# Kernel optimization log

Hardware: AMD Instinct MI355X
Metric: run time of the kernel (lower is better)

## Reference

```python
import jax, jax.numpy as jnp
import numpy as np

B, N, DQ, DK, DV = 8, 2048, 1024, 1024, 1024

def setup_inputs() -> dict:
    key = jax.random.key(0)
    kx, kq, kk, kv = jax.random.split(key, 4)
    x = jax.random.normal(kx, (B, N, DQ), dtype=jnp.float32)
    # nn.Linear(dim_q, dim_k, bias=False) weights: [out, in]
    s = 1.0 / np.sqrt(DQ)
    Wq = jax.random.uniform(kq, (DK, DQ), jnp.float32, -s, s)
    Wk = jax.random.uniform(kk, (DK, DQ), jnp.float32, -s, s)
    Wv = jax.random.uniform(kv, (DV, DQ), jnp.float32, -s, s)
    return {"x": x, "Wq": Wq, "Wk": Wk, "Wv": Wv}

def reference(x, Wq, Wk, Wv):
    batch, n, _ = x.shape
    q = jnp.einsum('bnd,kd->bnk', x, Wq)  # [B,n,DK]
    k = jnp.einsum('bnd,kd->bnk', x, Wk)  # [B,n,DK]
    v = jnp.einsum('bnd,vd->bnv', x, Wv)  # [B,n,DV]
    norm = 1.0 / jnp.sqrt(jnp.asarray(Wq.shape[0], jnp.float32))
    dist = jnp.einsum('bik,bjk->bij', q, k) * norm  # [B,n,n]
    causal = jnp.tril(jnp.ones((n, n), dtype=bool))
    dist = jnp.where(causal[None, :, :], dist, jnp.float32(-1e20))
    dist = jax.nn.softmax(dist, axis=-1)
    att = jnp.einsum('bij,bjv->biv', dist, v)  # [B,n,DV]
    return att
```

## Files before the change

### kernel.cpp

```cpp
#include <hip/hip_runtime.h>
#include <hip/hip_bf16.h>

#define BM 128
#define BN 128
#define BK 32
#define TILE_ELEMS (BM * BK)

typedef __attribute__((ext_vector_type(4))) float floatx4;
typedef __bf16 bf16x8 __attribute__((ext_vector_type(8)));
typedef unsigned int u32;
typedef unsigned short u16;

typedef __attribute__((address_space(1))) const u32 g_u32;
typedef __attribute__((address_space(3))) u32 l_u32;

__device__ __forceinline__ u16 f32_to_bf16(float f) {
    union { float f; u32 u; } x{f};
    u32 u = x.u;
    u32 r = (u + 0x7fffu + ((u >> 16) & 1u)) >> 16;
    return (u16)r;
}


__device__ __forceinline__ void stage_half_sw(const u16* gbase, u16* lds_half, int tid) {
    int lane = tid & 63;
    int rsub = lane >> 3;
    int colsw = ((lane & 7) ^ rsub) << 3;
#pragma unroll
    for (int j = 0; j < 2; ++j) {
        int q = (tid >> 6) * 2 + j;
        int row = q * 8 + rsub;
        const u16* g = gbase + row * 1024 + colsw;
        u16* l = lds_half + q * 512 + lane * 8;
        __builtin_amdgcn_global_load_lds((g_u32*)g, (l_u32*)l, 16, 0, 0);
    }
}

__global__ __launch_bounds__(512, 2)
void qkv_gemm8(const u16* __restrict__ A, const u16* __restrict__ Bw, u16* __restrict__ C)
{
    __shared__ u16 As[2][256 * 64];
    __shared__ u16 Bs[2][256 * 64];

    int bid = blockIdx.x;
    int wg = (bid & 7) * 96 + (bid >> 3);
    int mt = wg / 12, nt = wg - mt * 12;

    int tid = threadIdx.x;
    int lane = tid & 63, wv = tid >> 6;
    int wr = wv >> 2, wc = wv & 3;
    int lrow = lane & 15, quad = lane >> 4;
    int sw = lrow & 7;

    const u16* Ab = A + (long)mt * 256 * 1024;
    const u16* Bb = Bw + (long)nt * 256 * 1024;

    stage_half_sw(Bb,                  &Bs[0][0],        tid);
    stage_half_sw(Bb + 128 * 1024,     &Bs[0][128 * 64], tid);
    stage_half_sw(Ab,                  &As[0][0],        tid);
    stage_half_sw(Ab + 128 * 1024,     &As[0][128 * 64], tid);
    stage_half_sw(Bb + 64,             &Bs[1][0],        tid);
    stage_half_sw(Bb + 64 + 128 * 1024,&Bs[1][128 * 64], tid);
    asm volatile("s_waitcnt vmcnt(4)" ::: "memory");
    __builtin_amdgcn_sched_barrier(0);
    __builtin_amdgcn_s_barrier();

    floatx4 acc[8][4] = {};

    const int arow = (wr * 128 + lrow) * 64;
    const int brow = (wc * 64 + lrow) * 64;
    const int sl0 = (quad ^ sw) * 8;
    const int sl1 = ((4 + quad) ^ sw) * 8;

    for (int i = 0; i < 8; ++i) {
        int t1  = 2 * i + 1;
        int tn  = (2 * i + 2 <= 15) ? 2 * i + 2 : 15;
        int tn1 = (2 * i + 3 <= 15) ? 2 * i + 3 : 15;
        const u16* gA1 = Ab + t1 * 64;
        const u16* gB2 = Bb + tn * 64;
        const u16* gA2 = Ab + tn * 64;
        const u16* gB3 = Bb + tn1 * 64;

        bf16x8 bq0[4], bq1[4];
#pragma unroll
        for (int half = 0; half < 2; ++half) {
#pragma unroll
            for (int p = 0; p < 4; ++p) {
                if (p == 0) {
#pragma unroll
                    for (int ni = 0; ni < 4; ++ni) {
                        bq0[ni] = *(const bf16x8*)&Bs[half][brow + ni * 1024 + sl0];
                        bq1[ni] = *(const bf16x8*)&Bs[half][brow + ni * 1024 + sl1];
                    }
                }
                bf16x8 a00 = *(const bf16x8*)&As[half][arow + (2 * p)     * 1024 + sl0];
                bf16x8 a01 = *(const bf16x8*)&As[half][arow + (2 * p)     * 1024 + sl1];
                bf16x8 a10 = *(const bf16x8*)&As[half][arow + (2 * p + 1) * 1024 + sl0];
                bf16x8 a11 = *(const bf16x8*)&As[half][arow + (2 * p + 1) * 1024 + sl1];

                int ph = half * 4 + p;
                switch (ph) {
                    case 0: stage_half_sw(gA1,              &As[1][0],        tid); break;
                    case 1: stage_half_sw(gA1 + 128 * 1024, &As[1][128 * 64], tid); break;
                    case 2: stage_half_sw(gB2,              &Bs[0][0],        tid); break;
                    case 3: stage_half_sw(gB2 + 128 * 1024, &Bs[0][128 * 64], tid); break;
                    case 4: stage_half_sw(gA2,              &As[0][0],        tid); break;
                    case 5: stage_half_sw(gA2 + 128 * 1024, &As[0][128 * 64], tid); break;
                    case 6: stage_half_sw(gB3,              &Bs[1][0],        tid); break;
                    case 7: stage_half_sw(gB3 + 128 * 1024, &Bs[1][128 * 64], tid); break;
                }

                __builtin_amdgcn_s_barrier();
                __builtin_amdgcn_s_setprio(1);
                int m0 = 2 * p;
#pragma unroll
                for (int ni = 0; ni < 4; ++ni) {
                    acc[m0][ni]     = __builtin_amdgcn_mfma_f32_16x16x32_bf16(a00, bq0[ni], acc[m0][ni],     0, 0, 0);
                    acc[m0][ni]     = __builtin_amdgcn_mfma_f32_16x16x32_bf16(a01, bq1[ni], acc[m0][ni],     0, 0, 0);
                    acc[m0 + 1][ni] = __builtin_amdgcn_mfma_f32_16x16x32_bf16(a10, bq0[ni], acc[m0 + 1][ni], 0, 0, 0);
                    acc[m0 + 1][ni] = __builtin_amdgcn_mfma_f32_16x16x32_bf16(a11, bq1[ni], acc[m0 + 1][ni], 0, 0, 0);
                }
                __builtin_amdgcn_s_setprio(0);
                if (p == 3) {
                    asm volatile("s_waitcnt vmcnt(4)" ::: "memory");
                    __builtin_amdgcn_sched_barrier(0);
                }
                __builtin_amdgcn_s_barrier();
            }
        }
    }
    asm volatile("s_waitcnt vmcnt(0)" ::: "memory");
    __builtin_amdgcn_sched_barrier(0);

    long crow0 = (long)mt * 256 + wr * 128 + quad * 4;
    int  ccol0 = nt * 256 + wc * 64 + lrow;
#pragma unroll
    for (int mi = 0; mi < 8; ++mi) {
#pragma unroll
        for (int r = 0; r < 4; ++r) {
            long row = crow0 + mi * 16 + r;
#pragma unroll
            for (int ni = 0; ni < 4; ++ni) {
                int col = ccol0 + ni * 16;
                C[row * 3072 + col] = f32_to_bf16(acc[mi][ni][r]);
            }
        }
    }
}


__device__ __forceinline__ void stage_tile(const u16* gbase, int ld, u16* lds, int tid) {
#pragma unroll
    for (int it = 0; it < 2; ++it) {
        int flat = it * 2048 + tid * 8;
        int row = flat >> 5;
        int col = flat & 31;
        const u16* g = gbase + (long)row * ld + col;
        __builtin_amdgcn_global_load_lds((g_u32*)g, (l_u32*)(&lds[flat]), 16, 0, 0);
    }
}

template<bool OUT_BF16, int MODE>
__device__ __forceinline__ void gemm_body(
    const u16* __restrict__ Ab, const u16* __restrict__ Bb, void* __restrict__ Cb,
    int lda, int ldb, long ldc, int m0, int n0, int nkt, float scale,
    u16* As, u16* Bs, float* lsum)
{
    int tid = threadIdx.x;

    const u16* Arow = Ab + (long)m0 * lda;
    const u16* Brow = Bb + (long)n0 * ldb;

    stage_tile(Arow, lda, As, tid);
    stage_tile(Brow, ldb, Bs, tid);

    int wave = tid >> 6, lane = tid & 63;
    int wr = (wave >> 1) * 64, wc = (wave & 1) * 64;
    int lrow = lane & 15, quad = lane >> 4;

    floatx4 acc[4][4] = {};
    const int aoff = (wr + lrow) * BK + quad * 8;
    const int boff = (wc + lrow) * BK + quad * 8;

    for (int kt = 0; kt < nkt; ++kt) {
        __syncthreads();
        bf16x8 af[4], bfr[4];
#pragma unroll
        for (int i = 0; i < 4; ++i) {
            af[i]  = *(const bf16x8*)&As[aoff + i * 16 * BK];
            bfr[i] = *(const bf16x8*)&Bs[boff + i * 16 * BK];
        }
#pragma unroll
        for (int mi = 0; mi < 4; ++mi)
#pragma unroll
            for (int ni = 0; ni < 4; ++ni)
                acc[mi][ni] = __builtin_amdgcn_mfma_f32_16x16x32_bf16(af[mi], bfr[ni], acc[mi][ni], 0, 0, 0);
        __syncthreads();
        if (kt + 1 < nkt) {
            stage_tile(Arow + (kt + 1) * BK, lda, As, tid);
            stage_tile(Brow + (kt + 1) * BK, ldb, Bs, tid);
        }
    }

    long crow0 = m0 + wr + quad * 4;
    int  ccol0 = n0 + wc + lrow;
#pragma unroll
    for (int mi = 0; mi < 4; ++mi) {
#pragma unroll
        for (int r = 0; r < 4; ++r) {
            long row = crow0 + mi * 16 + r;
            float rs = 0.f;
            float linv = 1.f;
            if (MODE == 2) linv = 1.0f / lsum[row];
#pragma unroll
            for (int ni = 0; ni < 4; ++ni) {
                long col = ccol0 + ni * 16;
                float v = acc[mi][ni][r] * scale;
                if (MODE == 1) {
                    float e = (col > row) ? 0.f : __expf(v);
                    ((u16*)Cb)[row * ldc + col] = f32_to_bf16(e);
                    rs += e;
                } else if (MODE == 2) {
                    ((float*)Cb)[row * ldc + col] = v * linv;
                } else {
                    if (OUT_BF16) ((u16*)Cb)[row * ldc + col] = f32_to_bf16(v);
                    else          ((float*)Cb)[row * ldc + col] = v;
                }
            }
            if (MODE == 1) {
                rs += __shfl_xor(rs, 1, 16);
                rs += __shfl_xor(rs, 2, 16);
                rs += __shfl_xor(rs, 4, 16);
                rs += __shfl_xor(rs, 8, 16);
                if (lrow == 0) atomicAdd(&lsum[row], rs);
            }
        }
    }
}

__global__ __launch_bounds__(256)
void s_gemm(const u16* __restrict__ QKVi, u16* __restrict__ P, float* __restrict__ lsum)
{
    __shared__ u16 As[TILE_ELEMS];
    __shared__ u16 Bs[TILE_ELEMS];
    int b = blockIdx.x, u = blockIdx.y, v = blockIdx.z;
    int mt, nt;
    if (u <= v) { mt = v; nt = u; } else { mt = 15 - v; nt = u - v - 1; }
    const u16* Ab = QKVi + (long)b * 2048 * 3072;
    const u16* Bb = Ab + 1024;
    gemm_body<true, 1>(Ab, Bb, P + (long)b * 2048 * 2048, 3072, 3072, 2048,
                       mt * BM, nt * BN, 32, 0.03125f, As, Bs, lsum + b * 2048);
}

__global__ __launch_bounds__(256)
void pv_gemm(const u16* __restrict__ P, const u16* __restrict__ Vt,
             float* __restrict__ O, const float* __restrict__ lsum)
{
    __shared__ u16 As[TILE_ELEMS];
    __shared__ u16 Bs[TILE_ELEMS];
    int b = blockIdx.x, nt = blockIdx.y, mt = blockIdx.z;
    const u16* Ab = P + (long)b * 2048 * 2048;
    const u16* Bb = Vt + (long)b * 2048;
    gemm_body<false, 2>(Ab, Bb, O + (long)b * 2048 * 1024, 2048, 16384, 1024,
                        mt * BM, nt * BN, mt * 4 + 4, 1.0f, As, Bs,
                        (float*)lsum + b * 2048);
}

__global__ __launch_bounds__(256)
void cvt_f32_bf16(const float* __restrict__ src, u16* __restrict__ dst, long n)
{
    long idx = ((long)blockIdx.x * 256 + threadIdx.x) << 2;
    if (idx >= n) return;
    float4 f = *(const float4*)(src + idx);
    ushort4 o;
    o.x = f32_to_bf16(f.x); o.y = f32_to_bf16(f.y);
    o.z = f32_to_bf16(f.z); o.w = f32_to_bf16(f.w);
    *(ushort4*)(dst + idx) = o;
}

__global__ __launch_bounds__(256)
void cvt_w3(const float* __restrict__ Wq, const float* __restrict__ Wk,
            const float* __restrict__ Wv, u16* __restrict__ dst)
{
    int which = blockIdx.x >> 10;
    const float* src = which == 0 ? Wq : (which == 1 ? Wk : Wv);
    long base = (long)(blockIdx.x & 1023) * 1024 + threadIdx.x * 4;
    float4 f = *(const float4*)(src + base);
    ushort4 o;
    o.x = f32_to_bf16(f.x); o.y = f32_to_bf16(f.y);
    o.z = f32_to_bf16(f.z); o.w = f32_to_bf16(f.w);
    *(ushort4*)(dst + (long)which * 1048576 + base) = o;
}

__global__ __launch_bounds__(256)
void transpose_v(const u16* __restrict__ QKVi, u16* __restrict__ Vt)
{
    __shared__ u16 tile[64][64 + 8];
    int t0 = blockIdx.x * 64;
    int d0 = blockIdx.y * 64;
    int tid = threadIdx.x;
    int lr = tid >> 3, lc = (tid & 7) * 8;
#pragma unroll
    for (int p = 0; p < 2; ++p) {
        int tok = lr + p * 32;
        const u16* src = QKVi + (long)(t0 + tok) * 3072 + 2048 + d0 + lc;
        *(uint4*)&tile[tok][lc] = *(const uint4*)src;
    }
    __syncthreads();
#pragma unroll
    for (int p = 0; p < 2; ++p) {
        int dq = lr + p * 32;
        u16 vals[8];
#pragma unroll
        for (int i = 0; i < 8; ++i) vals[i] = tile[lc + i][dq];
        *(uint4*)(Vt + (long)(d0 + dq) * 16384 + t0 + lc) = *(const uint4*)vals;
    }
}

extern "C" void kernel_launch(void* const* d_in, const int* in_sizes, int n_in,
                              void* d_out, int out_size, void* d_ws, size_t ws_size,
                              hipStream_t stream)
{
    const int B = 8, N = 2048, D = 1024;
    const long MT = (long)B * N;
    const long nX = MT * D;
    const long nW = (long)D * D;

    const float* x  = (const float*)d_in[0];
    const float* Wq = (const float*)d_in[1];
    const float* Wk = (const float*)d_in[2];
    const float* Wv = (const float*)d_in[3];
    float* out = (float*)d_out;

    u16* wb   = (u16*)d_ws;
    u16* xb   = wb + 3 * nW;
    u16* QKVi = xb + nX;
    u16* P    = QKVi + 3 * nX;
    u16* Vt   = xb;
    float* lsum = (float*)wb;

    cvt_f32_bf16<<<(int)(nX / 1024), 256, 0, stream>>>(x, xb, nX);
    cvt_w3<<<3072, 256, 0, stream>>>(Wq, Wk, Wv, wb);

    qkv_gemm8<<<dim3(768, 1, 1), 512, 0, stream>>>(xb, wb, QKVi);

    hipMemsetAsync(lsum, 0, (size_t)B * N * sizeof(float), stream);
    transpose_v<<<dim3(256, 16, 1), 256, 0, stream>>>(QKVi, Vt);

    s_gemm<<<dim3(8, 17, 8), 256, 0, stream>>>(QKVi, P, lsum);

    pv_gemm<<<dim3(8, 8, 16), 256, 0, stream>>>(P, Vt, out, lsum);
}
```

Baseline: 375.8 us.

## Fuse V transpose into QKV GEMM epilogue and widen PV GEMM tiles

The QKV projection GEMM now writes Q/K into a compact 2048-wide buffer and writes V directly in transposed layout from its accumulators. This removes the separate transpose_v kernel and its extra read/write pass over V. The PV GEMM is replaced with a 512-thread kernel using 128x256 tiles, dispatched with the heaviest causal row blocks first. That halves redundant reads of P per output column tile, at the cost of more LDS per block. The transposed V stores are strided 8-byte writes, which may coalesce poorly.

```diff
diff --git a/kernel.cpp b/kernel.cpp
--- a/kernel.cpp
+++ b/kernel.cpp
@@ -37,7 +37,8 @@
 }
 
 __global__ __launch_bounds__(512, 2)
-void qkv_gemm8(const u16* __restrict__ A, const u16* __restrict__ Bw, u16* __restrict__ C)
+void qkv_gemm8(const u16* __restrict__ A, const u16* __restrict__ Bw,
+               u16* __restrict__ QKi, u16* __restrict__ Vt)
 {
     __shared__ u16 As[2][256 * 64];
     __shared__ u16 Bs[2][256 * 64];
@@ -132,17 +133,32 @@
     asm volatile("s_waitcnt vmcnt(0)" ::: "memory");
     __builtin_amdgcn_sched_barrier(0);
 
-    long crow0 = (long)mt * 256 + wr * 128 + quad * 4;
-    int  ccol0 = nt * 256 + wc * 64 + lrow;
-#pragma unroll
-    for (int mi = 0; mi < 8; ++mi) {
-#pragma unroll
-        for (int r = 0; r < 4; ++r) {
-            long row = crow0 + mi * 16 + r;
+    if (nt < 8) {
+        long crow0 = (long)mt * 256 + wr * 128 + quad * 4;
+        int  ccol0 = nt * 256 + wc * 64 + lrow;
+#pragma unroll
+        for (int mi = 0; mi < 8; ++mi) {
+#pragma unroll
+            for (int r = 0; r < 4; ++r) {
+                long row = crow0 + mi * 16 + r;
+#pragma unroll
+                for (int ni = 0; ni < 4; ++ni)
+                    QKi[row * 2048 + ccol0 + ni * 16] = f32_to_bf16(acc[mi][ni][r]);
+            }
+        }
+    } else {
+        int dv0   = (nt - 8) * 256 + wc * 64 + lrow;
+        long tok0 = (long)mt * 256 + wr * 128 + quad * 4;
+#pragma unroll
+        for (int mi = 0; mi < 8; ++mi) {
 #pragma unroll
             for (int ni = 0; ni < 4; ++ni) {
-                int col = ccol0 + ni * 16;
-                C[row * 3072 + col] = f32_to_bf16(acc[mi][ni][r]);
+                ushort4 o;
+                o.x = f32_to_bf16(acc[mi][ni][0]);
+                o.y = f32_to_bf16(acc[mi][ni][1]);
+                o.z = f32_to_bf16(acc[mi][ni][2]);
+                o.w = f32_to_bf16(acc[mi][ni][3]);
+                *(ushort4*)(Vt + (long)(dv0 + ni * 16) * 16384 + tok0 + mi * 16) = o;
             }
         }
     }
@@ -210,8 +226,6 @@
         for (int r = 0; r < 4; ++r) {
             long row = crow0 + mi * 16 + r;
             float rs = 0.f;
-            float linv = 1.f;
-            if (MODE == 2) linv = 1.0f / lsum[row];
 #pragma unroll
             for (int ni = 0; ni < 4; ++ni) {
                 long col = ccol0 + ni * 16;
@@ -220,8 +234,6 @@
                     float e = (col > row) ? 0.f : __expf(v);
                     ((u16*)Cb)[row * ldc + col] = f32_to_bf16(e);
                     rs += e;
-                } else if (MODE == 2) {
-                    ((float*)Cb)[row * ldc + col] = v * linv;
                 } else {
                     if (OUT_BF16) ((u16*)Cb)[row * ldc + col] = f32_to_bf16(v);
                     else          ((float*)Cb)[row * ldc + col] = v;
@@ -239,31 +251,94 @@
 }
 
 __global__ __launch_bounds__(256)
-void s_gemm(const u16* __restrict__ QKVi, u16* __restrict__ P, float* __restrict__ lsum)
+void s_gemm(const u16* __restrict__ QKi, u16* __restrict__ P, float* __restrict__ lsum)
 {
     __shared__ u16 As[TILE_ELEMS];
     __shared__ u16 Bs[TILE_ELEMS];
     int b = blockIdx.x, u = blockIdx.y, v = blockIdx.z;
     int mt, nt;
     if (u <= v) { mt = v; nt = u; } else { mt = 15 - v; nt = u - v - 1; }
-    const u16* Ab = QKVi + (long)b * 2048 * 3072;
+    const u16* Ab = QKi + (long)b * 2048 * 2048;
     const u16* Bb = Ab + 1024;
-    gemm_body<true, 1>(Ab, Bb, P + (long)b * 2048 * 2048, 3072, 3072, 2048,
+    gemm_body<true, 1>(Ab, Bb, P + (long)b * 2048 * 2048, 2048, 2048, 2048,
                        mt * BM, nt * BN, 32, 0.03125f, As, Bs, lsum + b * 2048);
 }
 
-__global__ __launch_bounds__(256)
-void pv_gemm(const u16* __restrict__ P, const u16* __restrict__ Vt,
-             float* __restrict__ O, const float* __restrict__ lsum)
-{
-    __shared__ u16 As[TILE_ELEMS];
-    __shared__ u16 Bs[TILE_ELEMS];
-    int b = blockIdx.x, nt = blockIdx.y, mt = blockIdx.z;
-    const u16* Ab = P + (long)b * 2048 * 2048;
-    const u16* Bb = Vt + (long)b * 2048;
-    gemm_body<false, 2>(Ab, Bb, O + (long)b * 2048 * 1024, 2048, 16384, 1024,
-                        mt * BM, nt * BN, mt * 4 + 4, 1.0f, As, Bs,
-                        (float*)lsum + b * 2048);
+__global__ __launch_bounds__(512)
+void pv_gemm2(const u16* __restrict__ P, const u16* __restrict__ Vt,
+              float* __restrict__ O, const float* __restrict__ lsum)
+{
+    __shared__ u16 As[128 * 32];
+    __shared__ u16 Bs[256 * 32];
+    int b = blockIdx.x, nt = blockIdx.y, mt = 15 - blockIdx.z;
+    const u16* Ab = P  + (long)b * 2048 * 2048 + (long)mt * 128 * 2048;
+    const u16* Bb = Vt + (long)b * 2048 + (long)nt * 256 * 16384;
+    float* Ob = O + (long)b * 2048 * 1024;
+    const float* ls = lsum + b * 2048;
+    int nkt = mt * 4 + 4;
+
+    int tid = threadIdx.x, lane = tid & 63, wave = tid >> 6;
+    int wr = wave >> 2, wc = wave & 3;
+    int lrow = lane & 15, quad = lane >> 4;
+
+    {
+        int flat = tid * 8, row = flat >> 5, col = flat & 31;
+        __builtin_amdgcn_global_load_lds((g_u32*)(Ab + (long)row * 2048 + col),
+                                         (l_u32*)&As[flat], 16, 0, 0);
+#pragma unroll
+        for (int it = 0; it < 2; ++it) {
+            int f2 = it * 4096 + tid * 8, r2 = f2 >> 5, c2 = f2 & 31;
+            __builtin_amdgcn_global_load_lds((g_u32*)(Bb + (long)r2 * 16384 + c2),
+                                             (l_u32*)&Bs[f2], 16, 0, 0);
+        }
+    }
+
+    floatx4 acc[4][4] = {};
+    const int aoff = (wr * 64 + lrow) * 32 + quad * 8;
+    const int boff = (wc * 64 + lrow) * 32 + quad * 8;
+
+    for (int kt = 0; kt < nkt; ++kt) {
+        __syncthreads();
+        bf16x8 af[4], bfr[4];
+#pragma unroll
+        for (int i = 0; i < 4; ++i) {
+            af[i]  = *(const bf16x8*)&As[aoff + i * 16 * 32];
+            bfr[i] = *(const bf16x8*)&Bs[boff + i * 16 * 32];
+        }
+#pragma unroll
+        for (int mi = 0; mi < 4; ++mi)
+#pragma unroll
+            for (int ni = 0; ni < 4; ++ni)
+                acc[mi][ni] = __builtin_amdgcn_mfma_f32_16x16x32_bf16(af[mi], bfr[ni], acc[mi][ni], 0, 0, 0);
+        __syncthreads();
+        if (kt + 1 < nkt) {
+            const u16* An = Ab + (kt + 1) * 32;
+            const u16* Bn = Bb + (kt + 1) * 32;
+            int flat = tid * 8, row = flat >> 5, col = flat & 31;
+            __builtin_amdgcn_global_load_lds((g_u32*)(An + (long)row * 2048 + col),
+                                             (l_u32*)&As[flat], 16, 0, 0);
+#pragma unroll
+            for (int it = 0; it < 2; ++it) {
+                int f2 = it * 4096 + tid * 8, r2 = f2 >> 5, c2 = f2 & 31;
+                __builtin_amdgcn_global_load_lds((g_u32*)(Bn + (long)r2 * 16384 + c2),
+                                                 (l_u32*)&Bs[f2], 16, 0, 0);
+            }
+        }
+    }
+
+    int crow0 = mt * 128 + wr * 64 + quad * 4;
+    int ccol0 = nt * 256 + wc * 64 + lrow;
+#pragma unroll
+    for (int mi = 0; mi < 4; ++mi) {
+#pragma unroll
+        for (int r = 0; r < 4; ++r) {
+            int row = crow0 + mi * 16 + r;
+            float linv = 1.0f / ls[row];
+#pragma unroll
+            for (int ni = 0; ni < 4; ++ni)
+                Ob[(long)row * 1024 + ccol0 + ni * 16] = acc[mi][ni][r] * linv;
+        }
+    }
 }
 
 __global__ __launch_bounds__(256)
@@ -292,31 +367,6 @@
     *(ushort4*)(dst + (long)which * 1048576 + base) = o;
 }
 
-__global__ __launch_bounds__(256)
-void transpose_v(const u16* __restrict__ QKVi, u16* __restrict__ Vt)
-{
-    __shared__ u16 tile[64][64 + 8];
-    int t0 = blockIdx.x * 64;
-    int d0 = blockIdx.y * 64;
-    int tid = threadIdx.x;
-    int lr = tid >> 3, lc = (tid & 7) * 8;
-#pragma unroll
-    for (int p = 0; p < 2; ++p) {
-        int tok = lr + p * 32;
-        const u16* src = QKVi + (long)(t0 + tok) * 3072 + 2048 + d0 + lc;
-        *(uint4*)&tile[tok][lc] = *(const uint4*)src;
-    }
-    __syncthreads();
-#pragma unroll
-    for (int p = 0; p < 2; ++p) {
-        int dq = lr + p * 32;
-        u16 vals[8];
-#pragma unroll
-        for (int i = 0; i < 8; ++i) vals[i] = tile[lc + i][dq];
-        *(uint4*)(Vt + (long)(d0 + dq) * 16384 + t0 + lc) = *(const uint4*)vals;
-    }
-}
-
 extern "C" void kernel_launch(void* const* d_in, const int* in_sizes, int n_in,
                               void* d_out, int out_size, void* d_ws, size_t ws_size,
                               hipStream_t stream)
@@ -334,20 +384,19 @@
 
     u16* wb   = (u16*)d_ws;
     u16* xb   = wb + 3 * nW;
-    u16* QKVi = xb + nX;
-    u16* P    = QKVi + 3 * nX;
-    u16* Vt   = xb;
+    u16* QKi  = xb + nX;
+    u16* Vt   = QKi + MT * 2048;
+    u16* P    = Vt + nX;
     float* lsum = (float*)wb;
 
     cvt_f32_bf16<<<(int)(nX / 1024), 256, 0, stream>>>(x, xb, nX);
     cvt_w3<<<3072, 256, 0, stream>>>(Wq, Wk, Wv, wb);
 
-    qkv_gemm8<<<dim3(768, 1, 1), 512, 0, stream>>>(xb, wb, QKVi);
+    qkv_gemm8<<<dim3(768, 1, 1), 512, 0, stream>>>(xb, wb, QKi, Vt);
 
     hipMemsetAsync(lsum, 0, (size_t)B * N * sizeof(float), stream);
-    transpose_v<<<dim3(256, 16, 1), 256, 0, stream>>>(QKVi, Vt);
-
-    s_gemm<<<dim3(8, 17, 8), 256, 0, stream>>>(QKVi, P, lsum);
-
-    pv_gemm<<<dim3(8, 8, 16), 256, 0, stream>>>(P, Vt, out, lsum);
-}
+
+    s_gemm<<<dim3(8, 17, 8), 256, 0, stream>>>(QKi, P, lsum);
+
+    pv_gemm2<<<dim3(8, 4, 16), 512, 0, stream>>>(P, Vt, out, lsum);
+}
```

Result: faster. 361.1 us (-3.9%).
